# Optimization experiments

Hardware: AMD Instinct MI355X
Metric: run time of the kernel (lower is better)

The kernel has to match this reference:

```python
import jax, jax.numpy as jnp
import numpy as np

B, N, D = 32, 512, 256
ITERATION_STEPS = 2


def setup_inputs() -> dict:
    key = jax.random.key(0)
    ks = jax.random.split(key, 20)
    node = jax.random.normal(ks[0], (B, N, D), dtype=jnp.float32)
    node_mask = jnp.ones((B, N), dtype=jnp.int32)
    graphs = [(jax.random.uniform(ks[1 + i], (B, N, N)) < 0.05).astype(jnp.int32)
              for i in range(6)]
    s = 0.02
    params = {
        'w_nw': jax.random.normal(ks[8], (D, 1)) * s,
        'b_nw': jnp.zeros((1,), jnp.float32),
        'w_self': jax.random.normal(ks[9], (D, D)) * s,
        'b_self': jnp.zeros((D,), jnp.float32),
        'w_arg1': jax.random.normal(ks[10], (D, D)) * s,
        'w_arg2': jax.random.normal(ks[11], (D, D)) * s,
        'w_arg3': jax.random.normal(ks[12], (D, D)) * s,
        'w_arg4': jax.random.normal(ks[13], (D, D)) * s,
        'w_punct': jax.random.normal(ks[14], (D, D)) * s,
        'w_punct_re': jax.random.normal(ks[15], (D, D)) * s,
    }
    return {'node': node, 'node_mask': node_mask,
            'arg_graph_1': graphs[0], 'arg_graph_2': graphs[1],
            'arg_graph_3': graphs[2], 'arg_graph_4': graphs[3],
            'punct_graph': graphs[4], 'punct_graph_re': graphs[5],
            **params}


def reference(node, node_mask, arg_graph_1, arg_graph_2, arg_graph_3, arg_graph_4,
              punct_graph, punct_graph_re,
              w_nw, b_nw, w_self, b_self,
              w_arg1, w_arg2, w_arg3, w_arg4, w_punct, w_punct_re):
    n = node.shape[1]
    diag = jnp.eye(n, dtype=node_mask.dtype)  # [N,N]
    # dd_graph: pairwise valid mask with zeroed diagonal, [B,N,N]
    dd = node_mask[:, None, :] * node_mask[:, :, None] * (1 - diag)
    G = jnp.stack([arg_graph_1, arg_graph_2, arg_graph_3, arg_graph_4,
                   punct_graph, punct_graph_re], 0) * dd[None]  # [6,B,N,N]
    Gf = G.astype(node.dtype)
    # neighbor count over all 6 edge types; replace 0 by 1 to avoid div-by-zero
    nn_num = Gf.sum(axis=(0, -1))  # [B,N]
    nn_num = jnp.where(nn_num >= 1, nn_num, jnp.ones_like(nn_num))
    W = jnp.stack([w_arg1, w_arg2, w_arg3, w_arg4, w_punct, w_punct_re], 0)  # [6,D,D]

    all_weight = []
    for _ in range(ITERATION_STEPS):
        # (1) node relatedness measure
        d_node_weight = jax.nn.sigmoid(node @ w_nw + b_nw)[..., 0]  # [B,N]
        all_weight.append(d_node_weight)
        self_node_info = node @ w_self + b_self  # [B,N,D]
        # (2) message propagation: per edge type k, project then aggregate
        proj = jnp.einsum('bnd,kde->kbne', node, W)            # [6,B,N,D]
        masked_w = d_node_weight[None, :, None, :] * Gf        # [6,B,N,N]
        agg = jnp.einsum('kbmn,kbne->bme', masked_w, proj)     # [B,N,D]
        # (3) update
        node = jax.nn.relu(self_node_info + agg / nn_num[..., None])
    return node, jnp.stack(all_weight, axis=1)  # [B,N,D], [B,steps,N]
```

## Files before the change

kernel.cpp:

```cpp
#include <hip/hip_runtime.h>

#define Bb 32
#define Nn 512
#define Dd 256
#define KC 1792
#define NR (Bb * Nn)

typedef __bf16 bf16x8 __attribute__((ext_vector_type(8)));
typedef float  f32x4  __attribute__((ext_vector_type(4)));
typedef int    i32x4  __attribute__((ext_vector_type(4)));
typedef unsigned short u16;

__device__ __forceinline__ u16 f2bf(float x){
  union { float f; unsigned u; } c; c.f = x;
  unsigned u = c.u;
  u += 0x7FFFu + ((u >> 16) & 1u);
  return (u16)(u >> 16);
}

__global__ __launch_bounds__(256) void k_prep(
    const float* __restrict__ wself,
    const float* __restrict__ w0, const float* __restrict__ w1,
    const float* __restrict__ w2, const float* __restrict__ w3,
    const float* __restrict__ w4, const float* __restrict__ w5,
    u16* __restrict__ wcatT){
  int e = blockIdx.x;
  const float* Ws[7] = {wself, w0, w1, w2, w3, w4, w5};
  for (int c = threadIdx.x; c < KC; c += 256){
    int g = c >> 8, j = c & 255;
    wcatT[(size_t)e*KC + c] = f2bf(Ws[g][j*Dd + e]);
  }
}

#define GLD(d, p, o) asm volatile("global_load_dwordx4 %0, %1, off offset:" #o \
                                  : "=v"(d) : "v"(p))

__global__ __launch_bounds__(256) void k_pack(
    const int* __restrict__ g0, const int* __restrict__ g1,
    const int* __restrict__ g2, const int* __restrict__ g3,
    const int* __restrict__ g4, const int* __restrict__ g5,
    const int* __restrict__ mask,
    unsigned* __restrict__ Gp, float* __restrict__ rs){
  int t = threadIdx.x, l = t & 63, wv = t >> 6;
  int r = blockIdx.x * 4 + wv;
  int b = r >> 9, m = r & 511;
  size_t off = (size_t)r * Nn + l * 4;
  const int* pm = mask + (size_t)b * Nn + l * 4;
  const int* pa = g0 + off; const int* pb = g1 + off; const int* pcx = g2 + off;
  const int* pd = g3 + off; const int* pe = g4 + off; const int* pf = g5 + off;

  i32x4 A0,A1,B0,B1,C0,C1,D0,D1,E0,E1,F0,F1,M0,M1;
  GLD(M0,pm,0);  GLD(M1,pm,1024);
  GLD(A0,pa,0);  GLD(A1,pa,1024);
  GLD(B0,pb,0);  GLD(B1,pb,1024);
  GLD(C0,pcx,0); GLD(C1,pcx,1024);
  GLD(D0,pd,0);  GLD(D1,pd,1024);
  GLD(E0,pe,0);  GLD(E1,pe,1024);
  GLD(F0,pf,0);  GLD(F1,pf,1024);
  asm volatile("s_waitcnt vmcnt(0)" ::: "memory");
  __builtin_amdgcn_sched_barrier(0);

  int s1 = (l & 1) * 4, s2 = ((l >> 1) & 1) * 8, s3 = ((l >> 2) & 1) * 16;
  unsigned dm0 = ((m >> 2) == l)      ? (1u << (m & 3)) : 0u;
  unsigned dm1 = ((m >> 2) == 64 + l) ? (1u << (m & 3)) : 0u;
  int stot = 0;
#define PK(G, MM, DM, k, h) {                                              \
    unsigned nib = (unsigned)((G[0] & MM[0]) | ((G[1] & MM[1]) << 1) |     \
                              ((G[2] & MM[2]) << 2) | ((G[3] & MM[3]) << 3)) \
                   & ~(DM);                                                \
    stot += __popc(nib);                                                   \
    unsigned v = nib << s1; v |= (unsigned)__shfl_xor((int)v, 1);          \
    v <<= s2;               v |= (unsigned)__shfl_xor((int)v, 2);          \
    v <<= s3;               v |= (unsigned)__shfl_xor((int)v, 4);          \
    if ((l & 7) == 0)                                                      \
      Gp[((size_t)(k) * NR + r) * 16 + (h) * 8 + (l >> 3)] = v; }
  PK(A0,M0,dm0,0,0) PK(A1,M1,dm1,0,1)
  PK(B0,M0,dm0,1,0) PK(B1,M1,dm1,1,1)
  PK(C0,M0,dm0,2,0) PK(C1,M1,dm1,2,1)
  PK(D0,M0,dm0,3,0) PK(D1,M1,dm1,3,1)
  PK(E0,M0,dm0,4,0) PK(E1,M1,dm1,4,1)
  PK(F0,M0,dm0,5,0) PK(F1,M1,dm1,5,1)
#undef PK
  #pragma unroll
  for (int o = 1; o < 64; o <<= 1) stot += __shfl_xor(stot, o);
  if (l == 0)
    rs[r] = mask[r] ? 1.0f / (float)(stot < 1 ? 1 : stot) : 0.0f;
}
#undef GLD

__global__ __launch_bounds__(256) void k_dw(
    const float* __restrict__ node, const int* __restrict__ mask,
    const float* __restrict__ wnw, const float* __restrict__ bnw,
    float* __restrict__ aw_out,
    u16* __restrict__ Nbf, u16* __restrict__ XT){
  __shared__ float tile[32][268];
  __shared__ float dws[32];
  int b = blockIdx.x >> 4, n0 = (blockIdx.x & 15) << 5;
  int t = threadIdx.x;
  int row = t >> 3, seg = t & 7;
  const float* src = node + ((size_t)(b * Nn + n0 + row)) * Dd + seg * 32;
  u16* zn = Nbf + ((size_t)(b * Nn + n0 + row)) * Dd + seg * 32;
  #pragma unroll
  for (int c = 0; c < 8; ++c){
    float4 v = ((const float4*)src)[c];
    tile[row][seg * 32 + c * 4 + 0] = v.x;
    tile[row][seg * 32 + c * 4 + 1] = v.y;
    tile[row][seg * 32 + c * 4 + 2] = v.z;
    tile[row][seg * 32 + c * 4 + 3] = v.w;
    ushort4 h;
    h.x = f2bf(v.x); h.y = f2bf(v.y); h.z = f2bf(v.z); h.w = f2bf(v.w);
    ((ushort4*)zn)[c] = h;
  }
  __syncthreads();
  float s = 0.f;
  #pragma unroll
  for (int c = 0; c < 32; ++c) s += tile[row][seg * 32 + c] * wnw[seg * 32 + c];
  s += __shfl_xor(s, 1); s += __shfl_xor(s, 2); s += __shfl_xor(s, 4);
  if (seg == 0){
    float dw = 1.f / (1.f + expf(-(s + bnw[0])));
    aw_out[b * (2 * Nn) + n0 + row] = dw;
    dws[row] = mask[b * Nn + n0 + row] ? dw : 0.f;
  }
  __syncthreads();
  #pragma unroll
  for (int p = 0; p < 4; ++p){
    int d = p * 64 + (t >> 2);
    int j0 = (t & 3) * 8;
    union { u16 h[8]; uint4 v; } pk;
    #pragma unroll
    for (int jj = 0; jj < 8; ++jj)
      pk.h[jj] = f2bf(dws[j0 + jj] * tile[j0 + jj][d]);
    *(uint4*)(XT + ((size_t)(b * Dd + d)) * Nn + n0 + j0) = pk.v;
  }
}

__global__ __launch_bounds__(256, 1) void k_fuse(
    const unsigned* __restrict__ Gp, const u16* __restrict__ XT,
    const u16* __restrict__ Nbf, const u16* __restrict__ wcatT,
    const float* __restrict__ rs, const float* __restrict__ bself,
    float* __restrict__ outp){
  __shared__ u16 As[64 * 72];
  __shared__ u16 BW[256 * 72];
  __shared__ u16 Ts[64 * 264];
  int mt = blockIdx.x, b = blockIdx.y, m0 = mt * 64;
  int t = threadIdx.x, lane = t & 63, wn = t >> 6;
  int arow = t >> 2, aq = t & 3;
  const u16* Xb = XT + (size_t)b * Dd * Nn;

  float rsv[16];
  #pragma unroll
  for (int i = 0; i < 4; ++i)
    #pragma unroll
    for (int r = 0; r < 4; ++r)
      rsv[i * 4 + r] = rs[b * Nn + m0 + i * 16 + (lane >> 4) * 4 + r];

  f32x4 accO[4][4];
  #pragma unroll
  for (int i = 0; i < 4; ++i)
    #pragma unroll
    for (int q = 0; q < 4; ++q) accO[i][q] = (f32x4){0.f, 0.f, 0.f, 0.f};

  for (int k = 0; k < 7; ++k){
    if (k < 6){
      const unsigned* Gr = Gp + ((size_t)k * NR + b * Nn + m0) * 16;
      unsigned wpre[8];
      #pragma unroll
      for (int ks = 0; ks < 8; ++ks)
        wpre[ks] = Gr[arow * 16 + ks * 2 + (aq >> 1)];
      f32x4 Ta[4][4];
      #pragma unroll
      for (int i = 0; i < 4; ++i)
        #pragma unroll
        for (int q = 0; q < 4; ++q) Ta[i][q] = (f32x4){0.f, 0.f, 0.f, 0.f};

      for (int ks = 0; ks < 8; ++ks){
        int k0 = ks * 64;
        {
          unsigned bits = (wpre[ks] >> ((aq & 1) * 16)) & 0xFFFFu;
          union { u16 h[16]; uint4 v[2]; } pk;
          #pragma unroll
          for (int c = 0; c < 16; ++c)
            pk.h[c] = ((bits >> c) & 1u) ? 0x3F80 : 0;
          *(uint4*)&As[arow * 72 + aq * 16]     = pk.v[0];
          *(uint4*)&As[arow * 72 + aq * 16 + 8] = pk.v[1];
        }
        #pragma unroll
        for (int p = 0; p < 8; ++p){
          int rowb = p * 32 + (t >> 3);
          *(uint4*)&BW[rowb * 72 + (t & 7) * 8] =
              *(const uint4*)(Xb + (size_t)rowb * Nn + k0 + (t & 7) * 8);
        }
        __syncthreads();
        #pragma unroll
        for (int kk = 0; kk < 2; ++kk){
          bf16x8 av[4], bv[4];
          #pragma unroll
          for (int i = 0; i < 4; ++i)
            av[i] = *(const bf16x8*)&As[(i * 16 + (lane & 15)) * 72 + kk * 32 + (lane >> 4) * 8];
          #pragma unroll
          for (int q = 0; q < 4; ++q)
            bv[q] = *(const bf16x8*)&BW[(wn * 64 + q * 16 + (lane & 15)) * 72 + kk * 32 + (lane >> 4) * 8];
          #pragma unroll
          for (int i = 0; i < 4; ++i)
            #pragma unroll
            for (int q = 0; q < 4; ++q)
              Ta[i][q] = __builtin_amdgcn_mfma_f32_16x16x32_bf16(av[i], bv[q], Ta[i][q], 0, 0, 0);
        }
        __syncthreads();
      }
      #pragma unroll
      for (int i = 0; i < 4; ++i)
        #pragma unroll
        for (int r = 0; r < 4; ++r){
          int row = i * 16 + (lane >> 4) * 4 + r;
          #pragma unroll
          for (int q = 0; q < 4; ++q)
            Ts[row * 264 + wn * 64 + q * 16 + (lane & 15)] =
                f2bf(Ta[i][q][r] * rsv[i * 4 + r]);
        }
      __syncthreads();
    } else {
      const u16* Nb = Nbf + ((size_t)(b * Nn + m0)) * Dd;
      #pragma unroll
      for (int p = 0; p < 8; ++p){
        int row = p * 8 + (t >> 5), col = (t & 31) * 8;
        *(uint4*)&Ts[row * 264 + col] = *(const uint4*)(Nb + (size_t)row * Dd + col);
      }
      __syncthreads();
    }
    int cb = (k < 6) ? (256 + k * 256) : 0;
    for (int cs = 0; cs < 4; ++cs){
      int c0 = cs * 64;
      #pragma unroll
      for (int p = 0; p < 8; ++p){
        int rowb = p * 32 + (t >> 3);
        *(uint4*)&BW[rowb * 72 + (t & 7) * 8] =
            *(const uint4*)(wcatT + (size_t)rowb * KC + cb + c0 + (t & 7) * 8);
      }
      __syncthreads();
      #pragma unroll
      for (int kk = 0; kk < 2; ++kk){
        bf16x8 av[4], bv[4];
        #pragma unroll
        for (int i = 0; i < 4; ++i)
          av[i] = *(const bf16x8*)&Ts[(i * 16 + (lane & 15)) * 264 + c0 + kk * 32 + (lane >> 4) * 8];
        #pragma unroll
        for (int q = 0; q < 4; ++q)
          bv[q] = *(const bf16x8*)&BW[(wn * 64 + q * 16 + (lane & 15)) * 72 + kk * 32 + (lane >> 4) * 8];
        #pragma unroll
        for (int i = 0; i < 4; ++i)
          #pragma unroll
          for (int q = 0; q < 4; ++q)
            accO[i][q] = __builtin_amdgcn_mfma_f32_16x16x32_bf16(av[i], bv[q], accO[i][q], 0, 0, 0);
      }
      __syncthreads();
    }
  }
  #pragma unroll
  for (int i = 0; i < 4; ++i){
    #pragma unroll
    for (int r = 0; r < 4; ++r){
      size_t gr = (size_t)b * Nn + m0 + i * 16 + (lane >> 4) * 4 + r;
      #pragma unroll
      for (int q = 0; q < 4; ++q){
        int e = wn * 64 + q * 16 + (lane & 15);
        float v = accO[i][q][r] + bself[e];
        outp[gr * Dd + e] = v > 0.f ? v : 0.f;
      }
    }
  }
}

extern "C" void kernel_launch(void* const* d_in, const int* in_sizes, int n_in,
                              void* d_out, int out_size, void* d_ws, size_t ws_size,
                              hipStream_t stream){
  (void)in_sizes; (void)n_in; (void)out_size; (void)ws_size;
  const float* node  = (const float*)d_in[0];
  const int*   mask  = (const int*)d_in[1];
  const int*   g[6];
  for (int i = 0; i < 6; ++i) g[i] = (const int*)d_in[2 + i];
  const float* wnw   = (const float*)d_in[8];
  const float* bnw   = (const float*)d_in[9];
  const float* wself = (const float*)d_in[10];
  const float* bself = (const float*)d_in[11];
  const float* W[6];
  for (int i = 0; i < 6; ++i) W[i] = (const float*)d_in[12 + i];

  float* out_node = (float*)d_out;
  float* out_aw   = out_node + (size_t)Bb * Nn * Dd;

  char* ws = (char*)d_ws;
  u16*      wcatT = (u16*)(ws);
  float*    rs    = (float*)(ws + 917504);
  unsigned* Gp    = (unsigned*)(ws + 1048576);
  u16*      XT    = (u16*)(ws + 7340032);
  u16*      Nbf   = (u16*)(ws + 15728640);

  k_prep<<<256, 256, 0, stream>>>(wself, W[0], W[1], W[2], W[3], W[4], W[5], wcatT);
  k_pack<<<4096, 256, 0, stream>>>(g[0], g[1], g[2], g[3], g[4], g[5], mask, Gp, rs);

  for (int t = 0; t < 2; ++t){
    const float* nsrc = (t == 0) ? node : out_node;
    k_dw<<<512, 256, 0, stream>>>(nsrc, mask, wnw, bnw, out_aw + t * Nn, Nbf, XT);
    k_fuse<<<dim3(8, 32), 256, 0, stream>>>(Gp, XT, Nbf, wcatT, rs, bself, out_node);
  }
}
```

Baseline: 260.2 us.

## Split fused edge-type loop across two blocks with partial-sum combine kernel

The fused kernel's seven-stage loop (six edge types plus the self projection) is now split across a new grid z dimension, so each (tile, batch) pair gets two blocks that handle 4 and 3 stages. The original grid had 256 blocks, which underfills the device; doubling it raises parallelism. Each block writes fp32 partial sums, and a new combine kernel adds them together with the bias and ReLU. The Ts shared tile drops its padding in favour of an XOR swizzle to avoid bank conflicts, and the one-block-per-CU launch bound is removed. The cost is an extra 16MB partial write plus a read and an extra launch per iteration.

```diff
diff --git a/kernel.cpp b/kernel.cpp
--- a/kernel.cpp
+++ b/kernel.cpp
@@ -17,6 +17,8 @@
   u += 0x7FFFu + ((u >> 16) & 1u);
   return (u16)(u >> 16);
 }
+
+#define TSW(row, col8) ((row) * 256 + (((col8) ^ ((row) & 7)) << 3))
 
 __global__ __launch_bounds__(256) void k_prep(
     const float* __restrict__ wself,
@@ -134,18 +136,18 @@
   }
 }
 
-__global__ __launch_bounds__(256, 1) void k_fuse(
+__global__ __launch_bounds__(256) void k_fuse(
     const unsigned* __restrict__ Gp, const u16* __restrict__ XT,
     const u16* __restrict__ Nbf, const u16* __restrict__ wcatT,
-    const float* __restrict__ rs, const float* __restrict__ bself,
-    float* __restrict__ outp){
+    const float* __restrict__ rs, float* __restrict__ part){
   __shared__ u16 As[64 * 72];
   __shared__ u16 BW[256 * 72];
-  __shared__ u16 Ts[64 * 264];
-  int mt = blockIdx.x, b = blockIdx.y, m0 = mt * 64;
+  __shared__ u16 Ts[64 * 256];
+  int mt = blockIdx.x, b = blockIdx.y, z = blockIdx.z, m0 = mt * 64;
   int t = threadIdx.x, lane = t & 63, wn = t >> 6;
   int arow = t >> 2, aq = t & 3;
   const u16* Xb = XT + (size_t)b * Dd * Nn;
+  float* myp = part + (size_t)z * ((size_t)NR * Dd);
 
   float rsv[16];
   #pragma unroll
@@ -160,7 +162,9 @@
     #pragma unroll
     for (int q = 0; q < 4; ++q) accO[i][q] = (f32x4){0.f, 0.f, 0.f, 0.f};
 
-  for (int k = 0; k < 7; ++k){
+  int nk = (z == 0) ? 4 : 3;
+  for (int ik = 0; ik < nk; ++ik){
+    int k = (z == 0) ? ((ik == 3) ? 6 : ik) : (3 + ik);
     if (k < 6){
       const unsigned* Gr = Gp + ((size_t)k * NR + b * Nn + m0) * 16;
       unsigned wpre[8];
@@ -214,17 +218,19 @@
         for (int r = 0; r < 4; ++r){
           int row = i * 16 + (lane >> 4) * 4 + r;
           #pragma unroll
-          for (int q = 0; q < 4; ++q)
-            Ts[row * 264 + wn * 64 + q * 16 + (lane & 15)] =
+          for (int q = 0; q < 4; ++q){
+            int col = wn * 64 + q * 16 + (lane & 15);
+            Ts[TSW(row, col >> 3) + (col & 7)] =
                 f2bf(Ta[i][q][r] * rsv[i * 4 + r]);
+          }
         }
       __syncthreads();
     } else {
       const u16* Nb = Nbf + ((size_t)(b * Nn + m0)) * Dd;
       #pragma unroll
       for (int p = 0; p < 8; ++p){
-        int row = p * 8 + (t >> 5), col = (t & 31) * 8;
-        *(uint4*)&Ts[row * 264 + col] = *(const uint4*)(Nb + (size_t)row * Dd + col);
+        int row = p * 8 + (t >> 5), col8 = t & 31;
+        *(uint4*)&Ts[TSW(row, col8)] = *(const uint4*)(Nb + (size_t)row * Dd + col8 * 8);
       }
       __syncthreads();
     }
@@ -242,8 +248,11 @@
       for (int kk = 0; kk < 2; ++kk){
         bf16x8 av[4], bv[4];
         #pragma unroll
-        for (int i = 0; i < 4; ++i)
-          av[i] = *(const bf16x8*)&Ts[(i * 16 + (lane & 15)) * 264 + c0 + kk * 32 + (lane >> 4) * 8];
+        for (int i = 0; i < 4; ++i){
+          int row = i * 16 + (lane & 15);
+          int col8 = ((c0 + kk * 32) >> 3) + (lane >> 4);
+          av[i] = *(const bf16x8*)&Ts[TSW(row, col8)];
+        }
         #pragma unroll
         for (int q = 0; q < 4; ++q)
           bv[q] = *(const bf16x8*)&BW[(wn * 64 + q * 16 + (lane & 15)) * 72 + kk * 32 + (lane >> 4) * 8];
@@ -264,11 +273,26 @@
       #pragma unroll
       for (int q = 0; q < 4; ++q){
         int e = wn * 64 + q * 16 + (lane & 15);
-        float v = accO[i][q][r] + bself[e];
-        outp[gr * Dd + e] = v > 0.f ? v : 0.f;
+        myp[gr * Dd + e] = accO[i][q][r];
       }
     }
   }
+}
+
+__global__ __launch_bounds__(256) void k_comb(
+    const float* __restrict__ part, const float* __restrict__ bself,
+    float* __restrict__ outp){
+  size_t i4 = (size_t)blockIdx.x * 256 + threadIdx.x;
+  const float4* p0 = (const float4*)part;
+  const float4* p1 = (const float4*)(part + (size_t)NR * Dd);
+  float4 a = p0[i4], bq = p1[i4];
+  float4 bias = *(const float4*)(bself + ((i4 * 4) & 255));
+  float4 v;
+  v.x = a.x + bq.x + bias.x; v.y = a.y + bq.y + bias.y;
+  v.z = a.z + bq.z + bias.z; v.w = a.w + bq.w + bias.w;
+  v.x = v.x > 0.f ? v.x : 0.f; v.y = v.y > 0.f ? v.y : 0.f;
+  v.z = v.z > 0.f ? v.z : 0.f; v.w = v.w > 0.f ? v.w : 0.f;
+  ((float4*)outp)[i4] = v;
 }
 
 extern "C" void kernel_launch(void* const* d_in, const int* in_sizes, int n_in,
@@ -295,6 +319,7 @@
   unsigned* Gp    = (unsigned*)(ws + 1048576);
   u16*      XT    = (u16*)(ws + 7340032);
   u16*      Nbf   = (u16*)(ws + 15728640);
+  float*    part  = (float*)(ws + 24117248);
 
   k_prep<<<256, 256, 0, stream>>>(wself, W[0], W[1], W[2], W[3], W[4], W[5], wcatT);
   k_pack<<<4096, 256, 0, stream>>>(g[0], g[1], g[2], g[3], g[4], g[5], mask, Gp, rs);
@@ -302,6 +327,7 @@
   for (int t = 0; t < 2; ++t){
     const float* nsrc = (t == 0) ? node : out_node;
     k_dw<<<512, 256, 0, stream>>>(nsrc, mask, wnw, bnw, out_aw + t * Nn, Nbf, XT);
-    k_fuse<<<dim3(8, 32), 256, 0, stream>>>(Gp, XT, Nbf, wcatT, rs, bself, out_node);
-  }
-}
+    k_fuse<<<dim3(8, 32, 2), 256, 0, stream>>>(Gp, XT, Nbf, wcatT, rs, part);
+    k_comb<<<4096, 256, 0, stream>>>(part, bself, out_node);
+  }
+}
```

After: 281.6 us. +8.2%, slower.

## Reorder to project-then-aggregate with separate projection GEMM and split aggregation

Applied to the files above, without the earlier changes.

Changes the contraction order. Each node is first projected per edge type (Y = (dw*X) @ W_k) in a new k_ycat GEMM kernel, and a new k_agg2 kernel then aggregates Y over the adjacency bitmasks and adds the self projection. This removes the Ts round-trip and the per-tile re-projection in the old fused kernel. It also doubles the grid through an output-column split with an XCD-aware block mapping. The cost is an extra launch and a large intermediate Yt buffer that goes through global memory, and the FLOP count stays similar.

```diff
diff --git a/kernel.cpp b/kernel.cpp
--- a/kernel.cpp
+++ b/kernel.cpp
@@ -92,7 +92,7 @@
     const float* __restrict__ node, const int* __restrict__ mask,
     const float* __restrict__ wnw, const float* __restrict__ bnw,
     float* __restrict__ aw_out,
-    u16* __restrict__ Nbf, u16* __restrict__ XT){
+    u16* __restrict__ Nbf, u16* __restrict__ Xp){
   __shared__ float tile[32][268];
   __shared__ float dws[32];
   int b = blockIdx.x >> 4, n0 = (blockIdx.x & 15) << 5;
@@ -122,30 +122,91 @@
     dws[row] = mask[b * Nn + n0 + row] ? dw : 0.f;
   }
   __syncthreads();
-  #pragma unroll
-  for (int p = 0; p < 4; ++p){
-    int d = p * 64 + (t >> 2);
-    int j0 = (t & 3) * 8;
-    union { u16 h[8]; uint4 v; } pk;
-    #pragma unroll
-    for (int jj = 0; jj < 8; ++jj)
-      pk.h[jj] = f2bf(dws[j0 + jj] * tile[j0 + jj][d]);
-    *(uint4*)(XT + ((size_t)(b * Dd + d)) * Nn + n0 + j0) = pk.v;
-  }
-}
-
-__global__ __launch_bounds__(256, 1) void k_fuse(
-    const unsigned* __restrict__ Gp, const u16* __restrict__ XT,
+  {
+    float dwr = dws[row];
+    u16* xp = Xp + ((size_t)(b * Nn + n0 + row)) * Dd + seg * 32;
+    #pragma unroll
+    for (int c = 0; c < 8; ++c){
+      ushort4 h;
+      h.x = f2bf(dwr * tile[row][seg * 32 + c * 4 + 0]);
+      h.y = f2bf(dwr * tile[row][seg * 32 + c * 4 + 1]);
+      h.z = f2bf(dwr * tile[row][seg * 32 + c * 4 + 2]);
+      h.w = f2bf(dwr * tile[row][seg * 32 + c * 4 + 3]);
+      ((ushort4*)xp)[c] = h;
+    }
+  }
+}
+
+__global__ __launch_bounds__(256) void k_ycat(
+    const u16* __restrict__ Xp, const u16* __restrict__ wcatT,
+    u16* __restrict__ Yt){
+  int n0 = blockIdx.x * 128, c0 = blockIdx.y * 128, b = blockIdx.z;
+  int kg = c0 >> 8, eg0 = c0 & 255;
+  __shared__ u16 As[128 * 72];
+  __shared__ u16 Bs[128 * 72];
+  int t = threadIdx.x, lane = t & 63, wid = t >> 6;
+  int wm = wid >> 1, wn = wid & 1;
+  f32x4 acc[4][4];
+  #pragma unroll
+  for (int i = 0; i < 4; ++i)
+    #pragma unroll
+    for (int q = 0; q < 4; ++q) acc[i][q] = (f32x4){0.f, 0.f, 0.f, 0.f};
+
+  for (int ks = 0; ks < 4; ++ks){
+    int k0 = ks * 64;
+    #pragma unroll
+    for (int p = 0; p < 4; ++p){
+      int row = p * 32 + (t >> 3);
+      *(uint4*)&As[row * 72 + (t & 7) * 8] =
+          *(const uint4*)(Xp + ((size_t)(b * Nn + n0 + row)) * Dd + k0 + (t & 7) * 8);
+      *(uint4*)&Bs[row * 72 + (t & 7) * 8] =
+          *(const uint4*)(wcatT + (size_t)(eg0 + row) * KC + 256 + kg * 256 + k0 + (t & 7) * 8);
+    }
+    __syncthreads();
+    #pragma unroll
+    for (int kk = 0; kk < 2; ++kk){
+      bf16x8 av[4], bv[4];
+      #pragma unroll
+      for (int i = 0; i < 4; ++i)
+        av[i] = *(const bf16x8*)&As[(wm * 64 + i * 16 + (lane & 15)) * 72 + kk * 32 + (lane >> 4) * 8];
+      #pragma unroll
+      for (int q = 0; q < 4; ++q)
+        bv[q] = *(const bf16x8*)&Bs[(wn * 64 + q * 16 + (lane & 15)) * 72 + kk * 32 + (lane >> 4) * 8];
+      #pragma unroll
+      for (int i = 0; i < 4; ++i)
+        #pragma unroll
+        for (int q = 0; q < 4; ++q)
+          acc[i][q] = __builtin_amdgcn_mfma_f32_16x16x32_bf16(av[i], bv[q], acc[i][q], 0, 0, 0);
+    }
+    __syncthreads();
+  }
+  #pragma unroll
+  for (int i = 0; i < 4; ++i){
+    int nbase = n0 + wm * 64 + i * 16 + (lane >> 4) * 4;
+    #pragma unroll
+    for (int q = 0; q < 4; ++q){
+      int eg = eg0 + wn * 64 + q * 16 + (lane & 15);
+      ushort4 h;
+      h.x = f2bf(acc[i][q][0]); h.y = f2bf(acc[i][q][1]);
+      h.z = f2bf(acc[i][q][2]); h.w = f2bf(acc[i][q][3]);
+      *(ushort4*)(Yt + ((size_t)((b * 6 + kg) * 256 + eg)) * Nn + nbase) = h;
+    }
+  }
+}
+
+__global__ __launch_bounds__(256) void k_agg2(
+    const unsigned* __restrict__ Gp, const u16* __restrict__ Yt,
     const u16* __restrict__ Nbf, const u16* __restrict__ wcatT,
     const float* __restrict__ rs, const float* __restrict__ bself,
     float* __restrict__ outp){
   __shared__ u16 As[64 * 72];
-  __shared__ u16 BW[256 * 72];
-  __shared__ u16 Ts[64 * 264];
-  int mt = blockIdx.x, b = blockIdx.y, m0 = mt * 64;
+  __shared__ u16 BW[128 * 72];
+  int id = blockIdx.x;
+  int xcd = id & 7, q = id >> 3;
+  int b = xcd * 4 + (q & 3), mt = (q >> 2) & 7, z = q >> 5;
+  int m0 = mt * 64, e0 = z * 128;
   int t = threadIdx.x, lane = t & 63, wn = t >> 6;
   int arow = t >> 2, aq = t & 3;
-  const u16* Xb = XT + (size_t)b * Dd * Nn;
 
   float rsv[16];
   #pragma unroll
@@ -154,118 +215,100 @@
     for (int r = 0; r < 4; ++r)
       rsv[i * 4 + r] = rs[b * Nn + m0 + i * 16 + (lane >> 4) * 4 + r];
 
-  f32x4 accO[4][4];
+  f32x4 accA[4][2], accS[4][2];
   #pragma unroll
   for (int i = 0; i < 4; ++i)
     #pragma unroll
-    for (int q = 0; q < 4; ++q) accO[i][q] = (f32x4){0.f, 0.f, 0.f, 0.f};
-
-  for (int k = 0; k < 7; ++k){
-    if (k < 6){
-      const unsigned* Gr = Gp + ((size_t)k * NR + b * Nn + m0) * 16;
-      unsigned wpre[8];
-      #pragma unroll
-      for (int ks = 0; ks < 8; ++ks)
-        wpre[ks] = Gr[arow * 16 + ks * 2 + (aq >> 1)];
-      f32x4 Ta[4][4];
-      #pragma unroll
-      for (int i = 0; i < 4; ++i)
-        #pragma unroll
-        for (int q = 0; q < 4; ++q) Ta[i][q] = (f32x4){0.f, 0.f, 0.f, 0.f};
-
-      for (int ks = 0; ks < 8; ++ks){
-        int k0 = ks * 64;
-        {
-          unsigned bits = (wpre[ks] >> ((aq & 1) * 16)) & 0xFFFFu;
-          union { u16 h[16]; uint4 v[2]; } pk;
-          #pragma unroll
-          for (int c = 0; c < 16; ++c)
-            pk.h[c] = ((bits >> c) & 1u) ? 0x3F80 : 0;
-          *(uint4*)&As[arow * 72 + aq * 16]     = pk.v[0];
-          *(uint4*)&As[arow * 72 + aq * 16 + 8] = pk.v[1];
-        }
-        #pragma unroll
-        for (int p = 0; p < 8; ++p){
-          int rowb = p * 32 + (t >> 3);
-          *(uint4*)&BW[rowb * 72 + (t & 7) * 8] =
-              *(const uint4*)(Xb + (size_t)rowb * Nn + k0 + (t & 7) * 8);
-        }
-        __syncthreads();
-        #pragma unroll
-        for (int kk = 0; kk < 2; ++kk){
-          bf16x8 av[4], bv[4];
-          #pragma unroll
-          for (int i = 0; i < 4; ++i)
-            av[i] = *(const bf16x8*)&As[(i * 16 + (lane & 15)) * 72 + kk * 32 + (lane >> 4) * 8];
-          #pragma unroll
-          for (int q = 0; q < 4; ++q)
-            bv[q] = *(const bf16x8*)&BW[(wn * 64 + q * 16 + (lane & 15)) * 72 + kk * 32 + (lane >> 4) * 8];
-          #pragma unroll
-          for (int i = 0; i < 4; ++i)
-            #pragma unroll
-            for (int q = 0; q < 4; ++q)
-              Ta[i][q] = __builtin_amdgcn_mfma_f32_16x16x32_bf16(av[i], bv[q], Ta[i][q], 0, 0, 0);
-        }
-        __syncthreads();
+    for (int q2 = 0; q2 < 2; ++q2){
+      accA[i][q2] = (f32x4){0.f, 0.f, 0.f, 0.f};
+      accS[i][q2] = (f32x4){0.f, 0.f, 0.f, 0.f};
+    }
+
+  for (int k = 0; k < 6; ++k){
+    const unsigned* Gr = Gp + ((size_t)k * NR + b * Nn + m0) * 16;
+    unsigned wpre[8];
+    #pragma unroll
+    for (int ks2 = 0; ks2 < 8; ++ks2)
+      wpre[ks2] = Gr[arow * 16 + ks2 * 2 + (aq >> 1)];
+    const u16* Yk = Yt + ((size_t)((b * 6 + k) * 256)) * Nn;
+
+    for (int ks2 = 0; ks2 < 8; ++ks2){
+      {
+        unsigned bits = (wpre[ks2] >> ((aq & 1) * 16)) & 0xFFFFu;
+        union { u16 h[16]; uint4 v[2]; } pk;
+        #pragma unroll
+        for (int c = 0; c < 16; ++c)
+          pk.h[c] = ((bits >> c) & 1u) ? 0x3F80 : 0;
+        *(uint4*)&As[arow * 72 + aq * 16]     = pk.v[0];
+        *(uint4*)&As[arow * 72 + aq * 16 + 8] = pk.v[1];
       }
       #pragma unroll
-      for (int i = 0; i < 4; ++i)
-        #pragma unroll
-        for (int r = 0; r < 4; ++r){
-          int row = i * 16 + (lane >> 4) * 4 + r;
-          #pragma unroll
-          for (int q = 0; q < 4; ++q)
-            Ts[row * 264 + wn * 64 + q * 16 + (lane & 15)] =
-                f2bf(Ta[i][q][r] * rsv[i * 4 + r]);
-        }
-      __syncthreads();
-    } else {
-      const u16* Nb = Nbf + ((size_t)(b * Nn + m0)) * Dd;
-      #pragma unroll
-      for (int p = 0; p < 8; ++p){
-        int row = p * 8 + (t >> 5), col = (t & 31) * 8;
-        *(uint4*)&Ts[row * 264 + col] = *(const uint4*)(Nb + (size_t)row * Dd + col);
+      for (int p = 0; p < 4; ++p){
+        int rowb = p * 32 + (t >> 3);
+        *(uint4*)&BW[rowb * 72 + (t & 7) * 8] =
+            *(const uint4*)(Yk + (size_t)(e0 + rowb) * Nn + ks2 * 64 + (t & 7) * 8);
       }
       __syncthreads();
-    }
-    int cb = (k < 6) ? (256 + k * 256) : 0;
-    for (int cs = 0; cs < 4; ++cs){
-      int c0 = cs * 64;
-      #pragma unroll
-      for (int p = 0; p < 8; ++p){
-        int rowb = p * 32 + (t >> 3);
-        *(uint4*)&BW[rowb * 72 + (t & 7) * 8] =
-            *(const uint4*)(wcatT + (size_t)rowb * KC + cb + c0 + (t & 7) * 8);
+      #pragma unroll
+      for (int kk = 0; kk < 2; ++kk){
+        bf16x8 av[4], bv[2];
+        #pragma unroll
+        for (int i = 0; i < 4; ++i)
+          av[i] = *(const bf16x8*)&As[(i * 16 + (lane & 15)) * 72 + kk * 32 + (lane >> 4) * 8];
+        #pragma unroll
+        for (int q2 = 0; q2 < 2; ++q2)
+          bv[q2] = *(const bf16x8*)&BW[(wn * 32 + q2 * 16 + (lane & 15)) * 72 + kk * 32 + (lane >> 4) * 8];
+        #pragma unroll
+        for (int i = 0; i < 4; ++i)
+          #pragma unroll
+          for (int q2 = 0; q2 < 2; ++q2)
+            accA[i][q2] = __builtin_amdgcn_mfma_f32_16x16x32_bf16(av[i], bv[q2], accA[i][q2], 0, 0, 0);
       }
       __syncthreads();
-      #pragma unroll
-      for (int kk = 0; kk < 2; ++kk){
-        bf16x8 av[4], bv[4];
-        #pragma unroll
-        for (int i = 0; i < 4; ++i)
-          av[i] = *(const bf16x8*)&Ts[(i * 16 + (lane & 15)) * 264 + c0 + kk * 32 + (lane >> 4) * 8];
-        #pragma unroll
-        for (int q = 0; q < 4; ++q)
-          bv[q] = *(const bf16x8*)&BW[(wn * 64 + q * 16 + (lane & 15)) * 72 + kk * 32 + (lane >> 4) * 8];
-        #pragma unroll
-        for (int i = 0; i < 4; ++i)
-          #pragma unroll
-          for (int q = 0; q < 4; ++q)
-            accO[i][q] = __builtin_amdgcn_mfma_f32_16x16x32_bf16(av[i], bv[q], accO[i][q], 0, 0, 0);
-      }
-      __syncthreads();
-    }
+    }
+  }
+  for (int ds = 0; ds < 4; ++ds){
+    #pragma unroll
+    for (int p = 0; p < 2; ++p){
+      int row = p * 32 + (t >> 3);
+      *(uint4*)&As[row * 72 + (t & 7) * 8] =
+          *(const uint4*)(Nbf + ((size_t)(b * Nn + m0 + row)) * Dd + ds * 64 + (t & 7) * 8);
+    }
+    #pragma unroll
+    for (int p = 0; p < 4; ++p){
+      int rowb = p * 32 + (t >> 3);
+      *(uint4*)&BW[rowb * 72 + (t & 7) * 8] =
+          *(const uint4*)(wcatT + (size_t)(e0 + rowb) * KC + ds * 64 + (t & 7) * 8);
+    }
+    __syncthreads();
+    #pragma unroll
+    for (int kk = 0; kk < 2; ++kk){
+      bf16x8 av[4], bv[2];
+      #pragma unroll
+      for (int i = 0; i < 4; ++i)
+        av[i] = *(const bf16x8*)&As[(i * 16 + (lane & 15)) * 72 + kk * 32 + (lane >> 4) * 8];
+      #pragma unroll
+      for (int q2 = 0; q2 < 2; ++q2)
+        bv[q2] = *(const bf16x8*)&BW[(wn * 32 + q2 * 16 + (lane & 15)) * 72 + kk * 32 + (lane >> 4) * 8];
+      #pragma unroll
+      for (int i = 0; i < 4; ++i)
+        #pragma unroll
+        for (int q2 = 0; q2 < 2; ++q2)
+          accS[i][q2] = __builtin_amdgcn_mfma_f32_16x16x32_bf16(av[i], bv[q2], accS[i][q2], 0, 0, 0);
+    }
+    __syncthreads();
   }
   #pragma unroll
   for (int i = 0; i < 4; ++i){
     #pragma unroll
     for (int r = 0; r < 4; ++r){
       size_t gr = (size_t)b * Nn + m0 + i * 16 + (lane >> 4) * 4 + r;
-      #pragma unroll
-      for (int q = 0; q < 4; ++q){
-        int e = wn * 64 + q * 16 + (lane & 15);
-        float v = accO[i][q][r] + bself[e];
-        outp[gr * Dd + e] = v > 0.f ? v : 0.f;
+      float rsm = rsv[i * 4 + r];
+      #pragma unroll
+      for (int q2 = 0; q2 < 2; ++q2){
+        int col = e0 + wn * 32 + q2 * 16 + (lane & 15);
+        float v = rsm * accA[i][q2][r] + accS[i][q2][r] + bself[col];
+        outp[gr * Dd + col] = v > 0.f ? v : 0.f;
       }
     }
   }
@@ -293,15 +336,17 @@
   u16*      wcatT = (u16*)(ws);
   float*    rs    = (float*)(ws + 917504);
   unsigned* Gp    = (unsigned*)(ws + 1048576);
-  u16*      XT    = (u16*)(ws + 7340032);
+  u16*      Xp    = (u16*)(ws + 7340032);
   u16*      Nbf   = (u16*)(ws + 15728640);
+  u16*      Yt    = (u16*)(ws + 24117248);
 
   k_prep<<<256, 256, 0, stream>>>(wself, W[0], W[1], W[2], W[3], W[4], W[5], wcatT);
   k_pack<<<4096, 256, 0, stream>>>(g[0], g[1], g[2], g[3], g[4], g[5], mask, Gp, rs);
 
   for (int t = 0; t < 2; ++t){
     const float* nsrc = (t == 0) ? node : out_node;
-    k_dw<<<512, 256, 0, stream>>>(nsrc, mask, wnw, bnw, out_aw + t * Nn, Nbf, XT);
-    k_fuse<<<dim3(8, 32), 256, 0, stream>>>(Gp, XT, Nbf, wcatT, rs, bself, out_node);
-  }
-}
+    k_dw<<<512, 256, 0, stream>>>(nsrc, mask, wnw, bnw, out_aw + t * Nn, Nbf, Xp);
+    k_ycat<<<dim3(4, 12, 32), 256, 0, stream>>>(Xp, wcatT, Yt);
+    k_agg2<<<512, 256, 0, stream>>>(Gp, Yt, Nbf, wcatT, rs, bself, out_node);
+  }
+}
```

After: 243.4 us. -6.5%, faster.
